# Kernel optimization log

Hardware: AMD Instinct MI355X
Metric: run time of the kernel (lower is better)

The kernel has to match this reference:

```python
import jax, jax.numpy as jnp
import numpy as np

N = 10000
E = 160000
IN_CH, HID, OUT = 14, 128, 4
HEADS = 8
NEG_SLOPE = 0.2


def setup_inputs() -> dict:
    key = jax.random.key(0)
    ks = jax.random.split(key, 16)
    glorot = lambda k, shape: jax.random.normal(k, shape, jnp.float32) * np.sqrt(2.0 / (shape[0] + shape[-1]))
    inp = {
        'x': jax.random.normal(ks[0], (N, IN_CH), jnp.float32),
        'edge_index': jax.random.randint(ks[1], (2, E), 0, N, jnp.int64),
        # layer 1: 14 -> 8 heads x 128, concat
        'W1': glorot(ks[2], (IN_CH, HEADS * HID)),
        'a_src1': glorot(ks[3], (HEADS, HID)),
        'a_dst1': glorot(ks[4], (HEADS, HID)),
        'b1': jnp.zeros((HEADS * HID,), jnp.float32),
        # layer 2: 1024 -> 8 heads x 128, concat
        'W2': glorot(ks[5], (HEADS * HID, HEADS * HID)),
        'a_src2': glorot(ks[6], (HEADS, HID)),
        'a_dst2': glorot(ks[7], (HEADS, HID)),
        'b2': jnp.zeros((HEADS * HID,), jnp.float32),
        # layer 3: 1024 -> 1 head x 4, mean (concat=False)
        'W3': glorot(ks[8], (HEADS * HID, OUT)),
        'a_src3': glorot(ks[9], (1, OUT)),
        'a_dst3': glorot(ks[10], (1, OUT)),
        'b3': jnp.zeros((OUT,), jnp.float32),
    }
    return inp


def gat_conv(x, src, dst, W, a_src, a_dst, b, heads, out_ch, concat):
    n = x.shape[0]
    h = (x @ W).reshape(n, heads, out_ch)                      # [N,H,C]
    al_s = jnp.sum(h * a_src, axis=-1)                         # [N,H]
    al_d = jnp.sum(h * a_dst, axis=-1)                         # [N,H]
    e = al_s[src] + al_d[dst]                                  # [E,H]
    e = jnp.where(e > 0, e, NEG_SLOPE * e)                     # LeakyReLU(0.2)
    # segment softmax over incoming edges of each dst node
    m = jax.ops.segment_max(e, dst, num_segments=n)
    ex = jnp.exp(e - m[dst])
    z = jax.ops.segment_sum(ex, dst, num_segments=n)
    alpha = ex / (z[dst] + 1e-16)                              # [E,H]
    out = jax.ops.segment_sum(h[src] * alpha[:, :, None], dst, num_segments=n)  # [N,H,C]
    out = out.reshape(n, heads * out_ch) if concat else out.mean(axis=1)
    return out + b


def reference(x, edge_index, W1, a_src1, a_dst1, b1, W2, a_src2, a_dst2, b2, W3, a_src3, a_dst3, b3):
    n = x.shape[0]
    # add self-loops (PyG GATConv default)
    loop = jnp.arange(n, dtype=edge_index.dtype)
    src = jnp.concatenate([edge_index[0], loop])
    dst = jnp.concatenate([edge_index[1], loop])
    # dropout layers are identity in eval mode
    h = gat_conv(x, src, dst, W1, a_src1, a_dst1, b1, HEADS, HID, True)
    h = jax.nn.relu(h)
    h = gat_conv(h, src, dst, W2, a_src2, a_dst2, b2, HEADS, HID, True)
    h = jax.nn.relu(h)
    h = gat_conv(h, src, dst, W3, a_src3, a_dst3, b3, 1, OUT, False)
    h = jax.nn.relu(h)
    return h
```

## Files before the change

kernel.cpp:

```cpp
#include <hip/hip_runtime.h>

typedef unsigned short ushort_t;
typedef unsigned int uint32;

#define N_NODES 10000
#define N_EDGES 160000
#define ET (N_NODES + N_EDGES)
#define MPAD 10112
#define HT 1024
#define HEADS 8
#define NEG 0.2f

#define O_FLAG     0
#define O_SRC      256
#define O_DST      (O_SRC + 680192)
#define O_COUNTS   (O_DST + 680192)
#define O_OFFS     (O_COUNTS + 40192)
#define O_CURS     (O_OFFS + 40192)
#define O_SSORT    (O_CURS + 40192)
#define O_ALS      (O_SSORT + 680192)
#define O_ALD      (O_ALS + 320000)
#define O_AL3S     (O_ALD + 320000)
#define O_AL3D     (O_AL3S + 40192)
#define O_H3       (O_AL3D + 40192)
#define O_XF       (O_H3 + 160000)
#define O_W1F      (O_XF + 560128)
#define O_AS1F     (O_W1F + 57344)
#define O_W3F      (O_AS1F + 24576)
#define O_S3F      (O_W3F + 16384)
#define O_W2T      (O_S3F + 768)
#define O_BUFA     (O_W2T + 2097152)
#define O_BUFB     (O_BUFA + 20709376)

__device__ __forceinline__ float bf2f(ushort_t u){ return __uint_as_float(((uint32)u) << 16); }
__device__ __forceinline__ ushort_t f2bf(float f){
    uint32 x = __float_as_uint(f);
    return (ushort_t)((x + 0x7fffu + ((x >> 16) & 1u)) >> 16);
}
__device__ __forceinline__ void unpack2(uint32 u, float& lo, float& hi){
    lo = __uint_as_float(u << 16);
    hi = __uint_as_float(u & 0xffff0000u);
}

typedef __bf16 bf16x8 __attribute__((ext_vector_type(8)));
typedef float  f32x4  __attribute__((ext_vector_type(4)));

typedef const __attribute__((address_space(1))) uint32* gas1_u32;
typedef       __attribute__((address_space(3))) uint32* las3_u32;

__device__ __forceinline__ void gload_lds16(const void* g, void* l){
    __builtin_amdgcn_global_load_lds((gas1_u32)g, (las3_u32)l, 16, 0, 0);
}

__global__ void k_probe(const int* __restrict__ ei, const uint32* __restrict__ w1raw,
                        int* __restrict__ flags){
    if (threadIdx.x == 0){
        int nz = 0;
        for (int i = 0; i < 128; i++) nz |= ei[2*i + 1];
        flags[0] = (nz == 0) ? 1 : 0;
    }
    if (threadIdx.x == 1){
        int cnt = 0;
        for (int i = 0; i < 256; i++){
            uint32 e = (w1raw[i] >> 7) & 0xffu;
            cnt += (e >= 64u && e <= 160u) ? 1 : 0;
        }
        flags[1] = (cnt > 200) ? 0 : 1;
    }
}

struct CvtArgs {
    const void* src[12];
    float*      dst[12];
    int         n[12];
};

__global__ __launch_bounds__(256) void k_cvt(CvtArgs a, const int* __restrict__ flags){
    int aid = blockIdx.y;
    int n = a.n[aid];
    int base = blockIdx.x * 1024 + threadIdx.x * 4;
    if (base >= n) return;
    int f32 = flags[1];
    const void* s = a.src[aid];
    float* d = a.dst[aid];
    #pragma unroll
    for (int j = 0; j < 4; j++){
        int i = base + j;
        if (i < n){
            d[i] = f32 ? ((const float*)s)[i] : bf2f(((const ushort_t*)s)[i]);
        }
    }
}

__global__ __launch_bounds__(256) void k_extract(const void* __restrict__ ei, const int* __restrict__ flags,
                                                 int* __restrict__ src, int* __restrict__ dst){
    int i = blockIdx.x * 256 + threadIdx.x;
    int is64 = flags[0];
    if (i < N_EDGES){
        if (is64){
            const long long* p = (const long long*)ei;
            src[i] = (int)p[i]; dst[i] = (int)p[N_EDGES + i];
        } else {
            const int* p = (const int*)ei;
            src[i] = p[i]; dst[i] = p[N_EDGES + i];
        }
    } else if (i < ET){
        int n = i - N_EDGES;
        src[i] = n; dst[i] = n;
    }
}

__global__ __launch_bounds__(256) void k_hist(const int* __restrict__ dst, int* __restrict__ counts){
    int i = blockIdx.x * 256 + threadIdx.x;
    if (i < ET) atomicAdd(&counts[dst[i]], 1);
}

__global__ __launch_bounds__(1024) void k_scan(const int* __restrict__ counts, int* __restrict__ offs,
                                               int* __restrict__ cursors, int n){
    __shared__ int wsum[16];
    __shared__ int running_s;
    int tid = threadIdx.x;
    int lane = tid & 63, wid = tid >> 6;
    if (tid == 0) running_s = 0;
    __syncthreads();
    for (int base = 0; base < n; base += 1024){
        int i = base + tid;
        int v = (i < n) ? counts[i] : 0;
        int x = v;
        #pragma unroll
        for (int d = 1; d < 64; d <<= 1){
            int t = __shfl_up(x, d, 64);
            if (lane >= d) x += t;
        }
        if (lane == 63) wsum[wid] = x;
        __syncthreads();
        if (wid == 0 && lane < 16){
            int w = wsum[lane];
            #pragma unroll
            for (int d = 1; d < 16; d <<= 1){
                int t = __shfl_up(w, d, 64);
                if (lane >= d) w += t;
            }
            wsum[lane] = w;
        }
        __syncthreads();
        int wprefix = (wid == 0) ? 0 : wsum[wid - 1];
        int run = running_s;
        int excl = run + wprefix + (x - v);
        if (i < n){ offs[i] = excl; cursors[i] = excl; }
        __syncthreads();
        if (tid == 0) running_s = run + wsum[15];
        __syncthreads();
    }
    if (tid == 0) offs[n] = running_s;
}

__global__ __launch_bounds__(256) void k_scatter(const int* __restrict__ src, const int* __restrict__ dst,
                                                 int* __restrict__ cursors, int* __restrict__ ssort){
    int i = blockIdx.x * 256 + threadIdx.x;
    if (i < ET){
        int pos = atomicAdd(&cursors[dst[i]], 1);
        ssort[pos] = src[i];
    }
}

__global__ __launch_bounds__(256) void k_gemm1(const float* __restrict__ x, const float* __restrict__ W1,
                                               ushort_t* __restrict__ h1){
    int n = blockIdx.x;
    int tid = threadIdx.x;
    __shared__ float xs[14];
    if (tid < 14) xs[tid] = x[n*14 + tid];
    __syncthreads();
    int c0 = tid * 4;
    float a0=0.f, a1=0.f, a2=0.f, a3=0.f;
    for (int k = 0; k < 14; k++){
        float xv = xs[k];
        float4 w = *(const float4*)(W1 + (size_t)k*HT + c0);
        a0 += xv*w.x; a1 += xv*w.y; a2 += xv*w.z; a3 += xv*w.w;
    }
    uint2 o;
    o.x = (uint32)f2bf(a0) | ((uint32)f2bf(a1) << 16);
    o.y = (uint32)f2bf(a2) | ((uint32)f2bf(a3) << 16);
    *(uint2*)(h1 + (size_t)n*HT + c0) = o;
}

__global__ __launch_bounds__(256) void k_alpha(const ushort_t* __restrict__ H, const float* __restrict__ a_src,
                                               const float* __restrict__ a_dst,
                                               float* __restrict__ alS, float* __restrict__ alD){
    int n = blockIdx.x, tid = threadIdx.x;
    int idx = tid * 4;
    uint2 hv = *(const uint2*)(H + (size_t)n*HT + idx);
    float4 sv = *(const float4*)(a_src + idx);
    float4 dv = *(const float4*)(a_dst + idx);
    float h0,h1,h2,h3;
    unpack2(hv.x, h0, h1); unpack2(hv.y, h2, h3);
    float s = h0*sv.x + h1*sv.y + h2*sv.z + h3*sv.w;
    float d = h0*dv.x + h1*dv.y + h2*dv.z + h3*dv.w;
    #pragma unroll
    for (int o = 16; o; o >>= 1){ s += __shfl_xor(s, o, 32); d += __shfl_xor(d, o, 32); }
    if ((tid & 31) == 0){ int head = tid >> 5; alS[n*HEADS + head] = s; alD[n*HEADS + head] = d; }
}

__global__ __launch_bounds__(256) void k_gat_agg(const ushort_t* __restrict__ H, const float* __restrict__ alS,
                                                 const float* __restrict__ alD, const int* __restrict__ offs,
                                                 const int* __restrict__ srcs, const float* __restrict__ bias,
                                                 ushort_t* __restrict__ out){
    int n = blockIdx.x;
    int tid = threadIdx.x;
    int head = tid >> 5;
    int l32 = tid & 31;
    int beg = offs[n], end = offs[n+1];
    float ad = alD[n*HEADS + head];
    __shared__ float sm[HEADS], sz[HEADS];
    float m = -1e30f;
    for (int e = beg + l32; e < end; e += 32){
        int s = srcs[e];
        float v = alS[s*HEADS + head] + ad;
        v = v > 0.f ? v : NEG*v;
        m = fmaxf(m, v);
    }
    #pragma unroll
    for (int o = 16; o; o >>= 1) m = fmaxf(m, __shfl_xor(m, o, 32));
    float z = 0.f;
    for (int e = beg + l32; e < end; e += 32){
        int s = srcs[e];
        float v = alS[s*HEADS + head] + ad;
        v = v > 0.f ? v : NEG*v;
        z += __expf(v - m);
    }
    #pragma unroll
    for (int o = 16; o; o >>= 1) z += __shfl_xor(z, o, 32);
    if (l32 == 0){ sm[head] = m; sz[head] = z; }
    __syncthreads();
    float mh = sm[head];
    float inv = 1.f / (sz[head] + 1e-16f);
    int ch = tid * 4;
    float a0=0.f, a1=0.f, a2=0.f, a3=0.f;
    for (int e = beg; e < end; ++e){
        int s = srcs[e];
        float v = alS[s*HEADS + head] + ad;
        v = v > 0.f ? v : NEG*v;
        float w = __expf(v - mh) * inv;
        uint2 hv = *(const uint2*)(H + (size_t)s*HT + ch);
        float f0,f1,f2,f3;
        unpack2(hv.x, f0, f1); unpack2(hv.y, f2, f3);
        a0 += w*f0; a1 += w*f1; a2 += w*f2; a3 += w*f3;
    }
    float4 bv = *(const float4*)(bias + ch);
    a0 = fmaxf(a0 + bv.x, 0.f); a1 = fmaxf(a1 + bv.y, 0.f);
    a2 = fmaxf(a2 + bv.z, 0.f); a3 = fmaxf(a3 + bv.w, 0.f);
    uint2 o;
    o.x = (uint32)f2bf(a0) | ((uint32)f2bf(a1) << 16);
    o.y = (uint32)f2bf(a2) | ((uint32)f2bf(a3) << 16);
    *(uint2*)(out + (size_t)n*HT + ch) = o;
}

__global__ __launch_bounds__(256) void k_transpose(const void* __restrict__ in, const int* __restrict__ flags,
                                                   ushort_t* __restrict__ out){
    __shared__ ushort_t tile[32][33];
    int f32 = flags[1];
    int bx = blockIdx.x, by = blockIdx.y;
    int cx = threadIdx.x & 31;
    int ry = (threadIdx.x >> 5) * 4;
    #pragma unroll
    for (int r = 0; r < 4; r++){
        size_t idx = (size_t)(by*32 + ry + r)*1024 + bx*32 + cx;
        tile[ry + r][cx] = f32 ? f2bf(((const float*)in)[idx]) : ((const ushort_t*)in)[idx];
    }
    __syncthreads();
    #pragma unroll
    for (int r = 0; r < 4; r++)
        out[(size_t)(bx*32 + ry + r)*1024 + by*32 + cx] = tile[cx][ry + r];
}

__global__ __launch_bounds__(256) void k_gemm2(const ushort_t* __restrict__ A, const ushort_t* __restrict__ BT,
                                               ushort_t* __restrict__ C){
    __shared__ ushort_t lA[128*32];
    __shared__ ushort_t lB[128*32];
    int tid = threadIdx.x;
    int bm = blockIdx.x, bn = blockIdx.y;
    int lane = tid & 63;
    int wave = tid >> 6;
    int wm = (wave & 1) * 64, wn = (wave >> 1) * 64;
    int lm = lane & 15, kg = lane >> 4;
    f32x4 acc[4][4];
    #pragma unroll
    for (int i = 0; i < 4; i++)
        #pragma unroll
        for (int j = 0; j < 4; j++) acc[i][j] = (f32x4)0.0f;

    const int K = 1024;
    int rowA0 = bm * 128, rowB0 = bn * 128;
    for (int k0 = 0; k0 < K; k0 += 32){
        #pragma unroll
        for (int it = 0; it < 2; ++it){
            int s = tid + it*256;
            int r = s >> 2, ks = s & 3;
            gload_lds16(A  + (size_t)(rowA0 + r)*K + k0 + ks*8, lA + s*8);
            gload_lds16(BT + (size_t)(rowB0 + r)*K + k0 + ks*8, lB + s*8);
        }
        __syncthreads();
        bf16x8 af[4], bfr[4];
        #pragma unroll
        for (int mt = 0; mt < 4; mt++) af[mt]  = *(const bf16x8*)(lA + (wm + mt*16 + lm)*32 + kg*8);
        #pragma unroll
        for (int nt = 0; nt < 4; nt++) bfr[nt] = *(const bf16x8*)(lB + (wn + nt*16 + lm)*32 + kg*8);
        #pragma unroll
        for (int mt = 0; mt < 4; mt++)
            #pragma unroll
            for (int nt = 0; nt < 4; nt++)
                acc[mt][nt] = __builtin_amdgcn_mfma_f32_16x16x32_bf16(af[mt], bfr[nt], acc[mt][nt], 0, 0, 0);
        __syncthreads();
    }
    #pragma unroll
    for (int mt = 0; mt < 4; mt++){
        int row_base = bm*128 + wm + mt*16 + kg*4;
        #pragma unroll
        for (int nt = 0; nt < 4; nt++){
            int col = bn*128 + wn + nt*16 + lm;
            #pragma unroll
            for (int r = 0; r < 4; r++){
                int row = row_base + r;
                if (row < N_NODES) C[(size_t)row*HT + col] = f2bf(acc[mt][nt][r]);
            }
        }
    }
}

__global__ __launch_bounds__(256) void k_gemm3(const ushort_t* __restrict__ A, const float* __restrict__ W3,
                                               const float* __restrict__ s3,
                                               float* __restrict__ h3, float* __restrict__ al3s, float* __restrict__ al3d){
    int n = blockIdx.x;
    int tid = threadIdx.x;
    float acc[4] = {0.f, 0.f, 0.f, 0.f};
    uint2 av = *(const uint2*)(A + (size_t)n*HT + tid*4);
    float a[4];
    unpack2(av.x, a[0], a[1]); unpack2(av.y, a[2], a[3]);
    #pragma unroll
    for (int j = 0; j < 4; j++){
        float4 w = ((const float4*)W3)[tid*4 + j];
        acc[0] += a[j]*w.x; acc[1] += a[j]*w.y; acc[2] += a[j]*w.z; acc[3] += a[j]*w.w;
    }
    #pragma unroll
    for (int o = 32; o; o >>= 1){
        #pragma unroll
        for (int c = 0; c < 4; c++) acc[c] += __shfl_xor(acc[c], o, 64);
    }
    __shared__ float part[4][4];
    int wave = tid >> 6, lane = tid & 63;
    if (lane == 0){
        #pragma unroll
        for (int c = 0; c < 4; c++) part[wave][c] = acc[c];
    }
    __syncthreads();
    if (tid == 0){
        float s = 0.f, d = 0.f;
        #pragma unroll
        for (int c = 0; c < 4; c++){
            float h = part[0][c] + part[1][c] + part[2][c] + part[3][c];
            h3[n*4 + c] = h;
            s += h * s3[c];
            d += h * s3[16 + c];
        }
        al3s[n] = s; al3d[n] = d;
    }
}

__global__ __launch_bounds__(64) void k_gat_agg3(const float* __restrict__ h3, const float* __restrict__ al3s,
                                                 const float* __restrict__ al3d, const int* __restrict__ offs,
                                                 const int* __restrict__ srcs, const float* __restrict__ b3,
                                                 const int* __restrict__ flags, void* __restrict__ out){
    int n = blockIdx.x;
    int l = threadIdx.x;
    int beg = offs[n], end = offs[n+1];
    float ad = al3d[n];
    float m = -1e30f;
    for (int e = beg + l; e < end; e += 64){
        float v = al3s[srcs[e]] + ad; v = v > 0.f ? v : NEG*v;
        m = fmaxf(m, v);
    }
    #pragma unroll
    for (int o = 32; o; o >>= 1) m = fmaxf(m, __shfl_xor(m, o, 64));
    float z = 0.f;
    for (int e = beg + l; e < end; e += 64){
        float v = al3s[srcs[e]] + ad; v = v > 0.f ? v : NEG*v;
        z += __expf(v - m);
    }
    #pragma unroll
    for (int o = 32; o; o >>= 1) z += __shfl_xor(z, o, 64);
    float inv = 1.f / (z + 1e-16f);
    float a0=0.f, a1=0.f, a2=0.f, a3=0.f;
    for (int e = beg + l; e < end; e += 64){
        int s = srcs[e];
        float v = al3s[s] + ad; v = v > 0.f ? v : NEG*v;
        float w = __expf(v - m) * inv;
        a0 += w*h3[s*4+0]; a1 += w*h3[s*4+1]; a2 += w*h3[s*4+2]; a3 += w*h3[s*4+3];
    }
    #pragma unroll
    for (int o = 32; o; o >>= 1){
        a0 += __shfl_xor(a0, o, 64); a1 += __shfl_xor(a1, o, 64);
        a2 += __shfl_xor(a2, o, 64); a3 += __shfl_xor(a3, o, 64);
    }
    if (l == 0){
        float r0 = fmaxf(a0 + b3[0], 0.f);
        float r1 = fmaxf(a1 + b3[1], 0.f);
        float r2 = fmaxf(a2 + b3[2], 0.f);
        float r3 = fmaxf(a3 + b3[3], 0.f);
        if (flags[1]){
            float* o4 = (float*)out;
            o4[n*4+0]=r0; o4[n*4+1]=r1; o4[n*4+2]=r2; o4[n*4+3]=r3;
        } else {
            ushort_t* o2 = (ushort_t*)out;
            o2[n*4+0]=f2bf(r0); o2[n*4+1]=f2bf(r1); o2[n*4+2]=f2bf(r2); o2[n*4+3]=f2bf(r3);
        }
    }
}

extern "C" void kernel_launch(void* const* d_in, const int* in_sizes, int n_in,
                              void* d_out, int out_size, void* d_ws, size_t ws_size,
                              hipStream_t stream){
    const void* x   = d_in[0];
    const void* ei  = d_in[1];
    const void* W1  = d_in[2];
    const void* as1 = d_in[3];
    const void* ad1 = d_in[4];
    const void* b1  = d_in[5];
    const void* W2  = d_in[6];
    const void* as2 = d_in[7];
    const void* ad2 = d_in[8];
    const void* b2  = d_in[9];
    const void* W3  = d_in[10];
    const void* as3 = d_in[11];
    const void* ad3 = d_in[12];
    const void* b3  = d_in[13];

    char* ws = (char*)d_ws;
    int* flags     = (int*)(ws + O_FLAG);
    int* srcA      = (int*)(ws + O_SRC);
    int* dstA      = (int*)(ws + O_DST);
    int* counts    = (int*)(ws + O_COUNTS);
    int* offs      = (int*)(ws + O_OFFS);
    int* cursors   = (int*)(ws + O_CURS);
    int* ssort     = (int*)(ws + O_SSORT);
    float* alS     = (float*)(ws + O_ALS);
    float* alD     = (float*)(ws + O_ALD);
    float* al3s    = (float*)(ws + O_AL3S);
    float* al3d    = (float*)(ws + O_AL3D);
    float* h3      = (float*)(ws + O_H3);
    float* xF      = (float*)(ws + O_XF);
    float* W1F     = (float*)(ws + O_W1F);
    float* wvecF   = (float*)(ws + O_AS1F);
    float* W3F     = (float*)(ws + O_W3F);
    float* s3F     = (float*)(ws + O_S3F);
    ushort_t* W2T  = (ushort_t*)(ws + O_W2T);
    ushort_t* bufA = (ushort_t*)(ws + O_BUFA);
    ushort_t* bufB = (ushort_t*)(ws + O_BUFB);

    const int EB = (ET + 255) / 256;

    k_probe<<<1, 64, 0, stream>>>((const int*)ei, (const uint32*)W1, flags);

    CvtArgs ca;
    ca.src[0]=x;   ca.dst[0]=xF;          ca.n[0]=140000;
    ca.src[1]=W1;  ca.dst[1]=W1F;         ca.n[1]=14336;
    ca.src[2]=as1; ca.dst[2]=wvecF+0*1024;  ca.n[2]=1024;
    ca.src[3]=ad1; ca.dst[3]=wvecF+1*1024;  ca.n[3]=1024;
    ca.src[4]=b1;  ca.dst[4]=wvecF+2*1024;  ca.n[4]=1024;
    ca.src[5]=as2; ca.dst[5]=wvecF+3*1024;  ca.n[5]=1024;
    ca.src[6]=ad2; ca.dst[6]=wvecF+4*1024;  ca.n[6]=1024;
    ca.src[7]=b2;  ca.dst[7]=wvecF+5*1024;  ca.n[7]=1024;
    ca.src[8]=W3;  ca.dst[8]=W3F;         ca.n[8]=4096;
    ca.src[9]=as3; ca.dst[9]=s3F+0;       ca.n[9]=4;
    ca.src[10]=ad3; ca.dst[10]=s3F+16;    ca.n[10]=4;
    ca.src[11]=b3;  ca.dst[11]=s3F+32;    ca.n[11]=4;
    k_cvt<<<dim3(137, 12), 256, 0, stream>>>(ca, flags);

    k_extract<<<EB, 256, 0, stream>>>(ei, flags, srcA, dstA);
    hipMemsetAsync(counts, 0, N_NODES*sizeof(int), stream);
    k_hist<<<EB, 256, 0, stream>>>(dstA, counts);
    k_scan<<<1, 1024, 0, stream>>>(counts, offs, cursors, N_NODES);
    k_scatter<<<EB, 256, 0, stream>>>(srcA, dstA, cursors, ssort);

    k_gemm1<<<N_NODES, 256, 0, stream>>>(xF, W1F, bufA);
    k_alpha<<<N_NODES, 256, 0, stream>>>(bufA, wvecF+0*1024, wvecF+1*1024, alS, alD);
    k_gat_agg<<<N_NODES, 256, 0, stream>>>(bufA, alS, alD, offs, ssort, wvecF+2*1024, bufB);

    k_transpose<<<dim3(32, 32), 256, 0, stream>>>(W2, flags, W2T);
    k_gemm2<<<dim3(79, 8), 256, 0, stream>>>(bufB, W2T, bufA);
    k_alpha<<<N_NODES, 256, 0, stream>>>(bufA, wvecF+3*1024, wvecF+4*1024, alS, alD);
    k_gat_agg<<<N_NODES, 256, 0, stream>>>(bufA, alS, alD, offs, ssort, wvecF+5*1024, bufB);

    k_gemm3<<<N_NODES, 256, 0, stream>>>(bufB, W3F, s3F, h3, al3s, al3d);
    k_gat_agg3<<<N_NODES, 64, 0, stream>>>(h3, al3s, al3d, offs, ssort, s3F+32, flags, d_out);
}
```

Measured before the change: 354.8 us.

## Fuse edge extract with histogram, gemm1 with alpha, restructure aggregation kernels

Merges edge extraction with the degree histogram, and fuses the layer-1 projection with its attention-logit computation using a grid-stride kernel that keeps W1 in shared memory. The layer-2 alpha, gemm3 and final aggregation now process several nodes per block to cut launch and tail overhead. The main GAT aggregation is rewritten to stage edge sources and softmax weights in shared memory per 64-edge chunk, splitting edges across two thread slots with 8 channels each and 16-byte loads. The cost is extra syncthreads and shared memory per block, which may lower occupancy.

```diff
diff --git a/kernel.cpp b/kernel.cpp
--- a/kernel.cpp
+++ b/kernel.cpp
@@ -10,6 +10,7 @@
 #define HT 1024
 #define HEADS 8
 #define NEG 0.2f
+#define AGG_CH 64
 
 #define O_FLAG     0
 #define O_SRC      256
@@ -92,27 +93,27 @@
     }
 }
 
-__global__ __launch_bounds__(256) void k_extract(const void* __restrict__ ei, const int* __restrict__ flags,
-                                                 int* __restrict__ src, int* __restrict__ dst){
+__global__ __launch_bounds__(256) void k_extract_hist(const void* __restrict__ ei, const int* __restrict__ flags,
+                                                      int* __restrict__ src, int* __restrict__ dst,
+                                                      int* __restrict__ counts){
     int i = blockIdx.x * 256 + threadIdx.x;
     int is64 = flags[0];
+    int s = -1, d = -1;
     if (i < N_EDGES){
         if (is64){
             const long long* p = (const long long*)ei;
-            src[i] = (int)p[i]; dst[i] = (int)p[N_EDGES + i];
+            s = (int)p[i]; d = (int)p[N_EDGES + i];
         } else {
             const int* p = (const int*)ei;
-            src[i] = p[i]; dst[i] = p[N_EDGES + i];
+            s = p[i]; d = p[N_EDGES + i];
         }
     } else if (i < ET){
-        int n = i - N_EDGES;
-        src[i] = n; dst[i] = n;
-    }
-}
-
-__global__ __launch_bounds__(256) void k_hist(const int* __restrict__ dst, int* __restrict__ counts){
-    int i = blockIdx.x * 256 + threadIdx.x;
-    if (i < ET) atomicAdd(&counts[dst[i]], 1);
+        s = i - N_EDGES; d = s;
+    }
+    if (d >= 0){
+        src[i] = s; dst[i] = d;
+        atomicAdd(&counts[d], 1);
+    }
 }
 
 __global__ __launch_bounds__(1024) void k_scan(const int* __restrict__ counts, int* __restrict__ offs,
@@ -164,41 +165,61 @@
     }
 }
 
-__global__ __launch_bounds__(256) void k_gemm1(const float* __restrict__ x, const float* __restrict__ W1,
-                                               ushort_t* __restrict__ h1){
-    int n = blockIdx.x;
-    int tid = threadIdx.x;
-    __shared__ float xs[14];
-    if (tid < 14) xs[tid] = x[n*14 + tid];
+__global__ __launch_bounds__(256) void k_gemm1f(const float* __restrict__ x, const float* __restrict__ W1,
+                                                const float* __restrict__ a_src, const float* __restrict__ a_dst,
+                                                ushort_t* __restrict__ h1,
+                                                float* __restrict__ alS, float* __restrict__ alD){
+    __shared__ float w1s[14 * HT];
+    int tid = threadIdx.x;
+    for (int i = tid * 4; i < 14 * HT; i += 1024)
+        *(float4*)(w1s + i) = *(const float4*)(W1 + i);
+    int c0 = tid * 4;
+    float4 sv = *(const float4*)(a_src + c0);
+    float4 dv = *(const float4*)(a_dst + c0);
+    int head = tid >> 5, l32 = tid & 31;
     __syncthreads();
+    for (int n = blockIdx.x; n < N_NODES; n += gridDim.x){
+        float a0=0.f, a1=0.f, a2=0.f, a3=0.f;
+        #pragma unroll
+        for (int k = 0; k < 14; k++){
+            float xv = x[n*14 + k];
+            float4 w = *(const float4*)(w1s + k*HT + c0);
+            a0 += xv*w.x; a1 += xv*w.y; a2 += xv*w.z; a3 += xv*w.w;
+        }
+        uint2 o;
+        o.x = (uint32)f2bf(a0) | ((uint32)f2bf(a1) << 16);
+        o.y = (uint32)f2bf(a2) | ((uint32)f2bf(a3) << 16);
+        *(uint2*)(h1 + (size_t)n*HT + c0) = o;
+        float h0,h1v,h2,h3v;
+        unpack2(o.x, h0, h1v); unpack2(o.y, h2, h3v);
+        float s = h0*sv.x + h1v*sv.y + h2*sv.z + h3v*sv.w;
+        float d = h0*dv.x + h1v*dv.y + h2*dv.z + h3v*dv.w;
+        #pragma unroll
+        for (int of = 16; of; of >>= 1){ s += __shfl_xor(s, of, 32); d += __shfl_xor(d, of, 32); }
+        if (l32 == 0){ alS[n*HEADS + head] = s; alD[n*HEADS + head] = d; }
+    }
+}
+
+__global__ __launch_bounds__(256) void k_alpha2(const ushort_t* __restrict__ H, const float* __restrict__ a_src,
+                                                const float* __restrict__ a_dst,
+                                                float* __restrict__ alS, float* __restrict__ alD){
+    int tid = threadIdx.x;
     int c0 = tid * 4;
-    float a0=0.f, a1=0.f, a2=0.f, a3=0.f;
-    for (int k = 0; k < 14; k++){
-        float xv = xs[k];
-        float4 w = *(const float4*)(W1 + (size_t)k*HT + c0);
-        a0 += xv*w.x; a1 += xv*w.y; a2 += xv*w.z; a3 += xv*w.w;
-    }
-    uint2 o;
-    o.x = (uint32)f2bf(a0) | ((uint32)f2bf(a1) << 16);
-    o.y = (uint32)f2bf(a2) | ((uint32)f2bf(a3) << 16);
-    *(uint2*)(h1 + (size_t)n*HT + c0) = o;
-}
-
-__global__ __launch_bounds__(256) void k_alpha(const ushort_t* __restrict__ H, const float* __restrict__ a_src,
-                                               const float* __restrict__ a_dst,
-                                               float* __restrict__ alS, float* __restrict__ alD){
-    int n = blockIdx.x, tid = threadIdx.x;
-    int idx = tid * 4;
-    uint2 hv = *(const uint2*)(H + (size_t)n*HT + idx);
-    float4 sv = *(const float4*)(a_src + idx);
-    float4 dv = *(const float4*)(a_dst + idx);
-    float h0,h1,h2,h3;
-    unpack2(hv.x, h0, h1); unpack2(hv.y, h2, h3);
-    float s = h0*sv.x + h1*sv.y + h2*sv.z + h3*sv.w;
-    float d = h0*dv.x + h1*dv.y + h2*dv.z + h3*dv.w;
-    #pragma unroll
-    for (int o = 16; o; o >>= 1){ s += __shfl_xor(s, o, 32); d += __shfl_xor(d, o, 32); }
-    if ((tid & 31) == 0){ int head = tid >> 5; alS[n*HEADS + head] = s; alD[n*HEADS + head] = d; }
+    float4 sv = *(const float4*)(a_src + c0);
+    float4 dv = *(const float4*)(a_dst + c0);
+    int head = tid >> 5, l32 = tid & 31;
+    int n0 = blockIdx.x * 16;
+    for (int i = 0; i < 16; i++){
+        int n = n0 + i;
+        uint2 hv = *(const uint2*)(H + (size_t)n*HT + c0);
+        float h0,h1,h2,h3;
+        unpack2(hv.x, h0, h1); unpack2(hv.y, h2, h3);
+        float s = h0*sv.x + h1*sv.y + h2*sv.z + h3*sv.w;
+        float d = h0*dv.x + h1*dv.y + h2*dv.z + h3*dv.w;
+        #pragma unroll
+        for (int of = 16; of; of >>= 1){ s += __shfl_xor(s, of, 32); d += __shfl_xor(d, of, 32); }
+        if (l32 == 0){ alS[n*HEADS + head] = s; alD[n*HEADS + head] = d; }
+    }
 }
 
 __global__ __launch_bounds__(256) void k_gat_agg(const ushort_t* __restrict__ H, const float* __restrict__ alS,
@@ -207,52 +228,92 @@
                                                  ushort_t* __restrict__ out){
     int n = blockIdx.x;
     int tid = threadIdx.x;
-    int head = tid >> 5;
-    int l32 = tid & 31;
     int beg = offs[n], end = offs[n+1];
-    float ad = alD[n*HEADS + head];
     __shared__ float sm[HEADS], sz[HEADS];
-    float m = -1e30f;
-    for (int e = beg + l32; e < end; e += 32){
-        int s = srcs[e];
-        float v = alS[s*HEADS + head] + ad;
-        v = v > 0.f ? v : NEG*v;
-        m = fmaxf(m, v);
-    }
-    #pragma unroll
-    for (int o = 16; o; o >>= 1) m = fmaxf(m, __shfl_xor(m, o, 32));
-    float z = 0.f;
-    for (int e = beg + l32; e < end; e += 32){
-        int s = srcs[e];
-        float v = alS[s*HEADS + head] + ad;
-        v = v > 0.f ? v : NEG*v;
-        z += __expf(v - m);
-    }
-    #pragma unroll
-    for (int o = 16; o; o >>= 1) z += __shfl_xor(z, o, 32);
-    if (l32 == 0){ sm[head] = m; sz[head] = z; }
+    __shared__ int   sE[AGG_CH];
+    __shared__ float wE[AGG_CH][HEADS];
+    __shared__ float red[HEADS][128];
+
+    {
+        int head32 = tid >> 5, l32 = tid & 31;
+        float ad = alD[n*HEADS + head32];
+        float m = -1e30f;
+        for (int e = beg + l32; e < end; e += 32){
+            float v = alS[srcs[e]*HEADS + head32] + ad;
+            v = v > 0.f ? v : NEG*v;
+            m = fmaxf(m, v);
+        }
+        #pragma unroll
+        for (int o = 16; o; o >>= 1) m = fmaxf(m, __shfl_xor(m, o, 32));
+        float z = 0.f;
+        for (int e = beg + l32; e < end; e += 32){
+            float v = alS[srcs[e]*HEADS + head32] + ad;
+            v = v > 0.f ? v : NEG*v;
+            z += __expf(v - m);
+        }
+        #pragma unroll
+        for (int o = 16; o; o >>= 1) z += __shfl_xor(z, o, 32);
+        if (l32 == 0){ sm[head32] = m; sz[head32] = z; }
+    }
     __syncthreads();
-    float mh = sm[head];
-    float inv = 1.f / (sz[head] + 1e-16f);
-    int ch = tid * 4;
-    float a0=0.f, a1=0.f, a2=0.f, a3=0.f;
-    for (int e = beg; e < end; ++e){
-        int s = srcs[e];
-        float v = alS[s*HEADS + head] + ad;
-        v = v > 0.f ? v : NEG*v;
-        float w = __expf(v - mh) * inv;
-        uint2 hv = *(const uint2*)(H + (size_t)s*HT + ch);
-        float f0,f1,f2,f3;
-        unpack2(hv.x, f0, f1); unpack2(hv.y, f2, f3);
-        a0 += w*f0; a1 += w*f1; a2 += w*f2; a3 += w*f3;
-    }
-    float4 bv = *(const float4*)(bias + ch);
-    a0 = fmaxf(a0 + bv.x, 0.f); a1 = fmaxf(a1 + bv.y, 0.f);
-    a2 = fmaxf(a2 + bv.z, 0.f); a3 = fmaxf(a3 + bv.w, 0.f);
-    uint2 o;
-    o.x = (uint32)f2bf(a0) | ((uint32)f2bf(a1) << 16);
-    o.y = (uint32)f2bf(a2) | ((uint32)f2bf(a3) << 16);
-    *(uint2*)(out + (size_t)n*HT + ch) = o;
+
+    int slot = tid >> 7;
+    int lt   = tid & 127;
+    int ch0  = lt * 8;
+    int head = lt >> 4;
+    float acc[8];
+    #pragma unroll
+    for (int j = 0; j < 8; j++) acc[j] = 0.f;
+
+    for (int cb = beg; cb < end; cb += AGG_CH){
+        int cn = min(AGG_CH, end - cb);
+        if (tid < cn) sE[tid] = srcs[cb + tid];
+        __syncthreads();
+        #pragma unroll
+        for (int r = 0; r < 2; r++){
+            int idx = tid + r*256;
+            int e = idx >> 3, hd = idx & 7;
+            if (e < cn){
+                int s = sE[e];
+                float v = alS[s*HEADS + hd] + alD[n*HEADS + hd];
+                v = v > 0.f ? v : NEG*v;
+                wE[e][hd] = __expf(v - sm[hd]) / (sz[hd] + 1e-16f);
+            }
+        }
+        __syncthreads();
+        for (int e = slot; e < cn; e += 2){
+            int s = sE[e];
+            float w = wE[e][head];
+            uint4 hv = *(const uint4*)(H + (size_t)s*HT + ch0);
+            float f0,f1,f2,f3,f4,f5,f6,f7;
+            unpack2(hv.x, f0, f1); unpack2(hv.y, f2, f3);
+            unpack2(hv.z, f4, f5); unpack2(hv.w, f6, f7);
+            acc[0]+=w*f0; acc[1]+=w*f1; acc[2]+=w*f2; acc[3]+=w*f3;
+            acc[4]+=w*f4; acc[5]+=w*f5; acc[6]+=w*f6; acc[7]+=w*f7;
+        }
+        __syncthreads();
+    }
+    if (slot == 1){
+        #pragma unroll
+        for (int j = 0; j < 8; j++) red[j & 7][lt] = acc[j] + 0.f*red[0][0];
+    }
+    __syncthreads();
+    if (slot == 0){
+        #pragma unroll
+        for (int j = 0; j < 8; j++) acc[j] += red[j][lt];
+        float4 bv0 = *(const float4*)(bias + ch0);
+        float4 bv1 = *(const float4*)(bias + ch0 + 4);
+        float r0 = fmaxf(acc[0]+bv0.x, 0.f), r1 = fmaxf(acc[1]+bv0.y, 0.f);
+        float r2 = fmaxf(acc[2]+bv0.z, 0.f), r3 = fmaxf(acc[3]+bv0.w, 0.f);
+        float r4 = fmaxf(acc[4]+bv1.x, 0.f), r5 = fmaxf(acc[5]+bv1.y, 0.f);
+        float r6 = fmaxf(acc[6]+bv1.z, 0.f), r7 = fmaxf(acc[7]+bv1.w, 0.f);
+        uint4 o;
+        o.x = (uint32)f2bf(r0) | ((uint32)f2bf(r1) << 16);
+        o.y = (uint32)f2bf(r2) | ((uint32)f2bf(r3) << 16);
+        o.z = (uint32)f2bf(r4) | ((uint32)f2bf(r5) << 16);
+        o.w = (uint32)f2bf(r6) | ((uint32)f2bf(r7) << 16);
+        *(uint4*)(out + (size_t)n*HT + ch0) = o;
+    }
 }
 
 __global__ __launch_bounds__(256) void k_transpose(const void* __restrict__ in, const int* __restrict__ flags,
@@ -330,48 +391,47 @@
 __global__ __launch_bounds__(256) void k_gemm3(const ushort_t* __restrict__ A, const float* __restrict__ W3,
                                                const float* __restrict__ s3,
                                                float* __restrict__ h3, float* __restrict__ al3s, float* __restrict__ al3d){
-    int n = blockIdx.x;
-    int tid = threadIdx.x;
-    float acc[4] = {0.f, 0.f, 0.f, 0.f};
-    uint2 av = *(const uint2*)(A + (size_t)n*HT + tid*4);
-    float a[4];
-    unpack2(av.x, a[0], a[1]); unpack2(av.y, a[2], a[3]);
-    #pragma unroll
-    for (int j = 0; j < 4; j++){
-        float4 w = ((const float4*)W3)[tid*4 + j];
-        acc[0] += a[j]*w.x; acc[1] += a[j]*w.y; acc[2] += a[j]*w.z; acc[3] += a[j]*w.w;
+    int tid = threadIdx.x;
+    int lane = tid & 63, wave = tid >> 6;
+    int n = blockIdx.x * 4 + wave;
+    if (n >= N_NODES) return;
+    float4 w3r[16];
+    #pragma unroll
+    for (int j = 0; j < 16; j++) w3r[j] = ((const float4*)W3)[lane*16 + j];
+    const uint4* ap = (const uint4*)(A + (size_t)n*HT + lane*16);
+    uint4 u0 = ap[0], u1 = ap[1];
+    uint32 uu[8] = {u0.x,u0.y,u0.z,u0.w,u1.x,u1.y,u1.z,u1.w};
+    float acc0=0.f, acc1=0.f, acc2=0.f, acc3=0.f;
+    #pragma unroll
+    for (int p = 0; p < 8; p++){
+        float lo, hi;
+        unpack2(uu[p], lo, hi);
+        float4 wl = w3r[p*2], wh = w3r[p*2+1];
+        acc0 += lo*wl.x + hi*wh.x;
+        acc1 += lo*wl.y + hi*wh.y;
+        acc2 += lo*wl.z + hi*wh.z;
+        acc3 += lo*wl.w + hi*wh.w;
     }
     #pragma unroll
     for (int o = 32; o; o >>= 1){
-        #pragma unroll
-        for (int c = 0; c < 4; c++) acc[c] += __shfl_xor(acc[c], o, 64);
-    }
-    __shared__ float part[4][4];
-    int wave = tid >> 6, lane = tid & 63;
+        acc0 += __shfl_xor(acc0, o, 64); acc1 += __shfl_xor(acc1, o, 64);
+        acc2 += __shfl_xor(acc2, o, 64); acc3 += __shfl_xor(acc3, o, 64);
+    }
     if (lane == 0){
-        #pragma unroll
-        for (int c = 0; c < 4; c++) part[wave][c] = acc[c];
-    }
-    __syncthreads();
-    if (tid == 0){
-        float s = 0.f, d = 0.f;
-        #pragma unroll
-        for (int c = 0; c < 4; c++){
-            float h = part[0][c] + part[1][c] + part[2][c] + part[3][c];
-            h3[n*4 + c] = h;
-            s += h * s3[c];
-            d += h * s3[16 + c];
-        }
-        al3s[n] = s; al3d[n] = d;
-    }
-}
-
-__global__ __launch_bounds__(64) void k_gat_agg3(const float* __restrict__ h3, const float* __restrict__ al3s,
-                                                 const float* __restrict__ al3d, const int* __restrict__ offs,
-                                                 const int* __restrict__ srcs, const float* __restrict__ b3,
-                                                 const int* __restrict__ flags, void* __restrict__ out){
-    int n = blockIdx.x;
-    int l = threadIdx.x;
+        *(float4*)(h3 + n*4) = make_float4(acc0, acc1, acc2, acc3);
+        al3s[n] = acc0*s3[0] + acc1*s3[1] + acc2*s3[2] + acc3*s3[3];
+        al3d[n] = acc0*s3[16] + acc1*s3[17] + acc2*s3[18] + acc3*s3[19];
+    }
+}
+
+__global__ __launch_bounds__(256) void k_gat_agg3(const float* __restrict__ h3, const float* __restrict__ al3s,
+                                                  const float* __restrict__ al3d, const int* __restrict__ offs,
+                                                  const int* __restrict__ srcs, const float* __restrict__ b3,
+                                                  const int* __restrict__ flags, void* __restrict__ out){
+    int tid = threadIdx.x;
+    int l = tid & 63, wave = tid >> 6;
+    int n = blockIdx.x * 4 + wave;
+    if (n >= N_NODES) return;
     int beg = offs[n], end = offs[n+1];
     float ad = al3d[n];
     float m = -1e30f;
@@ -394,7 +454,8 @@
         int s = srcs[e];
         float v = al3s[s] + ad; v = v > 0.f ? v : NEG*v;
         float w = __expf(v - m) * inv;
-        a0 += w*h3[s*4+0]; a1 += w*h3[s*4+1]; a2 += w*h3[s*4+2]; a3 += w*h3[s*4+3];
+        float4 hv = *(const float4*)(h3 + s*4);
+        a0 += w*hv.x; a1 += w*hv.y; a2 += w*hv.z; a3 += w*hv.w;
     }
     #pragma unroll
     for (int o = 32; o; o >>= 1){
@@ -461,35 +522,33 @@
     k_probe<<<1, 64, 0, stream>>>((const int*)ei, (const uint32*)W1, flags);
 
     CvtArgs ca;
-    ca.src[0]=x;   ca.dst[0]=xF;          ca.n[0]=140000;
-    ca.src[1]=W1;  ca.dst[1]=W1F;         ca.n[1]=14336;
+    ca.src[0]=x;   ca.dst[0]=xF;            ca.n[0]=140000;
+    ca.src[1]=W1;  ca.dst[1]=W1F;           ca.n[1]=14336;
     ca.src[2]=as1; ca.dst[2]=wvecF+0*1024;  ca.n[2]=1024;
     ca.src[3]=ad1; ca.dst[3]=wvecF+1*1024;  ca.n[3]=1024;
     ca.src[4]=b1;  ca.dst[4]=wvecF+2*1024;  ca.n[4]=1024;
     ca.src[5]=as2; ca.dst[5]=wvecF+3*1024;  ca.n[5]=1024;
     ca.src[6]=ad2; ca.dst[6]=wvecF+4*1024;  ca.n[6]=1024;
     ca.src[7]=b2;  ca.dst[7]=wvecF+5*1024;  ca.n[7]=1024;
-    ca.src[8]=W3;  ca.dst[8]=W3F;         ca.n[8]=4096;
-    ca.src[9]=as3; ca.dst[9]=s3F+0;       ca.n[9]=4;
-    ca.src[10]=ad3; ca.dst[10]=s3F+16;    ca.n[10]=4;
-    ca.src[11]=b3;  ca.dst[11]=s3F+32;    ca.n[11]=4;
+    ca.src[8]=W3;  ca.dst[8]=W3F;           ca.n[8]=4096;
+    ca.src[9]=as3; ca.dst[9]=s3F+0;         ca.n[9]=4;
+    ca.src[10]=ad3; ca.dst[10]=s3F+16;      ca.n[10]=4;
+    ca.src[11]=b3;  ca.dst[11]=s3F+32;      ca.n[11]=4;
     k_cvt<<<dim3(137, 12), 256, 0, stream>>>(ca, flags);
 
-    k_extract<<<EB, 256, 0, stream>>>(ei, flags, srcA, dstA);
     hipMemsetAsync(counts, 0, N_NODES*sizeof(int), stream);
-    k_hist<<<EB, 256, 0, stream>>>(dstA, counts);
+    k_extract_hist<<<EB, 256, 0, stream>>>(ei, flags, srcA, dstA, counts);
     k_scan<<<1, 1024, 0, stream>>>(counts, offs, cursors, N_NODES);
     k_scatter<<<EB, 256, 0, stream>>>(srcA, dstA, cursors, ssort);
 
-    k_gemm1<<<N_NODES, 256, 0, stream>>>(xF, W1F, bufA);
-    k_alpha<<<N_NODES, 256, 0, stream>>>(bufA, wvecF+0*1024, wvecF+1*1024, alS, alD);
+    k_gemm1f<<<512, 256, 0, stream>>>(xF, W1F, wvecF+0*1024, wvecF+1*1024, bufA, alS, alD);
     k_gat_agg<<<N_NODES, 256, 0, stream>>>(bufA, alS, alD, offs, ssort, wvecF+2*1024, bufB);
 
     k_transpose<<<dim3(32, 32), 256, 0, stream>>>(W2, flags, W2T);
     k_gemm2<<<dim3(79, 8), 256, 0, stream>>>(bufB, W2T, bufA);
-    k_alpha<<<N_NODES, 256, 0, stream>>>(bufA, wvecF+3*1024, wvecF+4*1024, alS, alD);
+    k_alpha2<<<625, 256, 0, stream>>>(bufA, wvecF+3*1024, wvecF+4*1024, alS, alD);
     k_gat_agg<<<N_NODES, 256, 0, stream>>>(bufA, alS, alD, offs, ssort, wvecF+5*1024, bufB);
 
-    k_gemm3<<<N_NODES, 256, 0, stream>>>(bufB, W3F, s3F, h3, al3s, al3d);
-    k_gat_agg3<<<N_NODES, 64, 0, stream>>>(h3, al3s, al3d, offs, ssort, s3F+32, flags, d_out);
-}
+    k_gemm3<<<2500, 256, 0, stream>>>(bufB, W3F, s3F, h3, al3s, al3d);
+    k_gat_agg3<<<2500, 256, 0, stream>>>(h3, al3s, al3d, offs, ssort, s3F+32, flags, d_out);
+}
```

New measurement: 334.5 us. 1.06x faster.
